# Optimization experiments

Hardware: AMD Instinct MI355X
Metric: run time of the kernel (lower is better)

The kernel has to match this reference:

```python
import jax, jax.numpy as jnp
import numpy as np

N, E, D = 50000, 800000, 128
NODE_IN, EDGE_IN, STEPS = 19, 4, 5
EPS = 1e-5

def leaky(x):
    return jnp.where(x > 0, x, 0.05 * x)

def mlp3(x, W1, b1, W2, b2, W3, b3):
    x = leaky(x @ W1 + b1)
    x = leaky(x @ W2 + b2)
    return x @ W3 + b3

def layer_norm(x, g, b):
    m = jnp.mean(x, axis=-1, keepdims=True)
    v = jnp.var(x, axis=-1, keepdims=True)
    return (x - m) * jax.lax.rsqrt(v + EPS) * g + b

def batch_norm(x, g, b):
    # training-mode BatchNorm1d: biased batch stats over node dim
    m = jnp.mean(x, axis=0)
    v = jnp.var(x, axis=0)
    return (x - m) * jax.lax.rsqrt(v + EPS) * g + b

def gcn_conv(x, src, dst, W, b):
    # PyG GCNConv: add self loops, sym-normalize by deg^{-1/2}, aggregate at dst
    h = x @ W  # [N, D]
    deg = jax.ops.segment_sum(jnp.ones(E, x.dtype), dst, num_segments=N) + 1.0
    dis = jax.lax.rsqrt(deg)
    msg = h[src] * (dis[src] * dis[dst])[:, None]  # [E, D]
    agg = jax.ops.segment_sum(msg, dst, num_segments=N) + h * (dis * dis)[:, None]
    return agg + b


def setup_inputs() -> dict:
    key = jax.random.key(0)
    ks = iter(jax.random.split(key, 64))
    w = lambda shape: jax.random.normal(next(ks), shape, jnp.float32) * 0.05
    z = lambda: jnp.zeros((D,), jnp.float32)
    o = lambda: jnp.ones((D,), jnp.float32)
    inp = {
        'node_feat': jax.random.normal(next(ks), (N, NODE_IN), jnp.float32),
        'edge_feat': jax.random.normal(next(ks), (E, EDGE_IN), jnp.float32),
        'edge_index': jax.random.randint(next(ks), (2, E), 0, N, jnp.int32),
        'enc_node_W1': w((NODE_IN, D)), 'enc_node_b1': z(),
        'enc_node_W2': w((D, D)), 'enc_node_b2': z(),
        'enc_node_W3': w((D, D)), 'enc_node_b3': z(),
        'enc_node_ln_g': o(), 'enc_node_ln_b': z(),
        'enc_edge_W1': w((EDGE_IN, D)), 'enc_edge_b1': z(),
        'enc_edge_W2': w((D, D)), 'enc_edge_b2': z(),
        'enc_edge_W3': w((D, D)), 'enc_edge_b3': z(),
        'enc_edge_ln_g': o(), 'enc_edge_ln_b': z(),
        'proc_W': w((STEPS, 2, D, D)),
        'proc_b': jnp.zeros((STEPS, 2, D), jnp.float32),
        'proc_bn_g': jnp.ones((STEPS, D), jnp.float32),
        'proc_bn_b': jnp.zeros((STEPS, D), jnp.float32),
        'dec_W1': w((D, D)), 'dec_b1': z(),
        'dec_W2': w((D, D)), 'dec_b2': z(),
        'dec_W3': w((D, D)), 'dec_b3': z(),
        'dec_ln_g': o(), 'dec_ln_b': z(),
    }
    return inp


def reference(node_feat, edge_feat, edge_index,
              enc_node_W1, enc_node_b1, enc_node_W2, enc_node_b2, enc_node_W3, enc_node_b3,
              enc_node_ln_g, enc_node_ln_b,
              enc_edge_W1, enc_edge_b1, enc_edge_W2, enc_edge_b2, enc_edge_W3, enc_edge_b3,
              enc_edge_ln_g, enc_edge_ln_b,
              proc_W, proc_b, proc_bn_g, proc_bn_b,
              dec_W1, dec_b1, dec_W2, dec_b2, dec_W3, dec_b3, dec_ln_g, dec_ln_b):
    src, dst = edge_index[0], edge_index[1]
    # encode
    hn = layer_norm(mlp3(node_feat, enc_node_W1, enc_node_b1, enc_node_W2, enc_node_b2,
                         enc_node_W3, enc_node_b3), enc_node_ln_g, enc_node_ln_b)
    he = layer_norm(mlp3(edge_feat, enc_edge_W1, enc_edge_b1, enc_edge_W2, enc_edge_b2,
                         enc_edge_W3, enc_edge_b3), enc_edge_ln_g, enc_edge_ln_b)
    # scatter-mean edge features onto source nodes
    cnt = jax.ops.segment_sum(jnp.ones(E, hn.dtype), src, num_segments=N)
    hn = hn + jax.ops.segment_sum(he, src, num_segments=N) / jnp.maximum(cnt, 1.0)[:, None]
    # 5 residual GCN processor steps (GCNConv -> LeakyReLU -> BN -> GCNConv)
    for s in range(STEPS):
        x = gcn_conv(hn, src, dst, proc_W[s, 0], proc_b[s, 0])
        x = batch_norm(leaky(x), proc_bn_g[s], proc_bn_b[s])
        x = gcn_conv(x, src, dst, proc_W[s, 1], proc_b[s, 1])
        hn = hn + x
    # decode
    return layer_norm(mlp3(hn, dec_W1, dec_b1, dec_W2, dec_b2, dec_W3, dec_b3),
                      dec_ln_g, dec_ln_b)
```

## Files before the change

kernel.cpp:

```cpp
#include <hip/hip_runtime.h>

#define NN 50000
#define NE 800000
#define DD 128
#define LN_EPS 1e-5f

typedef __attribute__((ext_vector_type(8))) short v8s;
typedef __attribute__((ext_vector_type(4))) unsigned v4u;
typedef __attribute__((ext_vector_type(4))) float f32x4;

union CvtHL { v4u u; v8s s; };

__device__ __forceinline__ float leakyf(float x){ return x > 0.f ? x : 0.05f*x; }
__device__ __forceinline__ short f2bf(float f){
  unsigned u = __float_as_uint(f);
  u = (u + 0x7fffu + ((u >> 16) & 1u)) >> 16;
  return (short)u;
}
__device__ __forceinline__ float bf2f(unsigned short h){
  return __uint_as_float(((unsigned)h) << 16);
}
__device__ __forceinline__ unsigned cvt_pk_bf16(float a, float b){
  unsigned r;
  asm("v_cvt_pk_bf16_f32 %0, %1, %2" : "=v"(r) : "v"(a), "v"(b));
  return r;
}
__device__ __forceinline__ unsigned pack_hi16(unsigned u0, unsigned u1){
  return __builtin_amdgcn_perm(u1, u0, 0x07060302u);
}
__device__ __forceinline__ short2 f2bf2v(float v){
  unsigned u = __float_as_uint(v);
  short hi = (short)(u >> 16);
  float lo = v - __uint_as_float(u & 0xffff0000u);
  return make_short2(hi, f2bf(lo));
}

__global__ void pack_w_kernel(const float* __restrict__ W, short* __restrict__ Wh,
                              short* __restrict__ Wl, int K, int Kp)
{
  int idx = blockIdx.x*256 + threadIdx.x;
  if (idx >= Kp*128) return;
  int k = idx >> 7, n = idx & 127;
  float v = (k < K) ? W[k*128 + n] : 0.f;
  short2 t = f2bf2v(v);
  size_t o = ((size_t)(k >> 3)*128 + n)*8 + (k & 7);
  Wh[o] = t.x; Wl[o] = t.y;
}

#define NPACK 11
struct PackArgs { const float* src[NPACK]; short* dh[NPACK]; short* dl[NPACK]; };

__global__ void pack_many_kernel(PackArgs pa)
{
  int m = blockIdx.y;
  int idx = blockIdx.x*256 + threadIdx.x;
  int k = idx >> 7, n = idx & 127;
  float v = pa.src[m][k*128 + n];
  short2 t = f2bf2v(v);
  size_t o = ((size_t)(k >> 3)*128 + n)*8 + (k & 7);
  pa.dh[m][o] = t.x; pa.dl[m][o] = t.y;
}

#define MFMA3(ah, al, bh, bl, ac) \
  ac = __builtin_amdgcn_mfma_f32_16x16x32_bf16(al, bh, ac, 0,0,0); \
  ac = __builtin_amdgcn_mfma_f32_16x16x32_bf16(ah, bl, ac, 0,0,0); \
  ac = __builtin_amdgcn_mfma_f32_16x16x32_bf16(ah, bh, ac, 0,0,0);

#define MFMA2(ah, bh, bl, ac) \
  ac = __builtin_amdgcn_mfma_f32_16x16x32_bf16(ah, bl, ac, 0,0,0); \
  ac = __builtin_amdgcn_mfma_f32_16x16x32_bf16(ah, bh, ac, 0,0,0);

#define SPLIT8(f0, f1, h, l) { \
  unsigned u0=__float_as_uint(f0.x), u1=__float_as_uint(f0.y), u2=__float_as_uint(f0.z), u3=__float_as_uint(f0.w); \
  unsigned u4=__float_as_uint(f1.x), u5=__float_as_uint(f1.y), u6=__float_as_uint(f1.z), u7=__float_as_uint(f1.w); \
  CvtHL ch_, cl_; \
  ch_.u = (v4u){ pack_hi16(u0,u1), pack_hi16(u2,u3), pack_hi16(u4,u5), pack_hi16(u6,u7) }; \
  cl_.u = (v4u){ \
    cvt_pk_bf16(f0.x-__uint_as_float(u0&0xffff0000u), f0.y-__uint_as_float(u1&0xffff0000u)), \
    cvt_pk_bf16(f0.z-__uint_as_float(u2&0xffff0000u), f0.w-__uint_as_float(u3&0xffff0000u)), \
    cvt_pk_bf16(f1.x-__uint_as_float(u4&0xffff0000u), f1.y-__uint_as_float(u5&0xffff0000u)), \
    cvt_pk_bf16(f1.z-__uint_as_float(u6&0xffff0000u), f1.w-__uint_as_float(u7&0xffff0000u)) }; \
  h = ch_.s; l = cl_.s; }

template<int IN_W, bool SCATTER>
__global__ __launch_bounds__(256)
void mlp_mfma_kernel(const float* __restrict__ x, int nrows,
                     const short* __restrict__ W1h, const short* __restrict__ W1l,
                     const float* __restrict__ b1,
                     const short* __restrict__ W2h, const short* __restrict__ W2l,
                     const float* __restrict__ b2,
                     const short* __restrict__ W3h, const short* __restrict__ W3l,
                     const float* __restrict__ b3,
                     const float* __restrict__ g, const float* __restrict__ bb,
                     float* __restrict__ out,
                     const int* __restrict__ sidx,
                     const int* __restrict__ eperm)
{
  constexpr int L1K = (IN_W + 31) / 32;
  __shared__ __align__(16) short Hh[128*136];
  __shared__ float lnS[128][2], lnQ[128][2];
  __shared__ int sidx_s[128];
  __shared__ __align__(16) uint4 xstage[SCATTER ? 128 : 1];

  const int tid  = threadIdx.x;
  const int lane = tid & 63, wave = tid >> 6;
  const int wr = wave >> 1, wc = wave & 1;
  const int quad = lane >> 4, low = lane & 15;
  const int row0 = blockIdx.x * 128;

  if (SCATTER) {
    if (tid < 128) {
      int e = eperm[row0 + tid];
      float4 f = ((const float4*)x)[e];
      unsigned u0=__float_as_uint(f.x), u1=__float_as_uint(f.y);
      unsigned u2=__float_as_uint(f.z), u3=__float_as_uint(f.w);
      uint4 st;
      st.x = pack_hi16(u0,u1);
      st.y = pack_hi16(u2,u3);
      st.z = cvt_pk_bf16(f.x-__uint_as_float(u0&0xffff0000u), f.y-__uint_as_float(u1&0xffff0000u));
      st.w = cvt_pk_bf16(f.z-__uint_as_float(u2&0xffff0000u), f.w-__uint_as_float(u3&0xffff0000u));
      xstage[tid] = st;
      sidx_s[tid] = sidx[row0 + tid];
    }
    __syncthreads();
  }

  f32x4 acc[4][4];

  #pragma unroll
  for (int tm=0;tm<4;tm++)
    #pragma unroll
    for (int tn=0;tn<4;tn++) acc[tm][tn] = (f32x4)0.f;

  for (int ks = 0; ks < L1K; ks++) {
    v8s ah[4], al[4], bh[4], bl[4];
    #pragma unroll
    for (int tm=0;tm<4;tm++) {
      int lr = wr*64 + tm*16 + low;
      v8s h = (v8s)0, l = (v8s)0;
      if (SCATTER && IN_W == 4) {
        if (quad == 0) {
          uint4 st = xstage[lr];
          CvtHL ch_, cl_;
          ch_.u = (v4u){ st.x, st.y, 0u, 0u };
          cl_.u = (v4u){ st.z, st.w, 0u, 0u };
          h = ch_.s; l = cl_.s;
        }
      } else if (IN_W % 32 == 0) {
        int r = row0 + lr;
        if (r < nrows) {
          const float* p = x + (size_t)r*IN_W + ks*32 + quad*8;
          float4 f0 = *(const float4*)p;
          float4 f1 = *(const float4*)(p + 4);
          SPLIT8(f0, f1, h, l);
        }
      } else {
        int r = row0 + lr;
        #pragma unroll
        for (int j=0;j<8;j++) {
          int k = ks*32 + quad*8 + j;
          if (k < IN_W && r < nrows) {
            short2 t = f2bf2v(x[(size_t)r*IN_W + k]);
            h[j] = t.x; l[j] = t.y;
          }
        }
      }
      ah[tm] = h; al[tm] = l;
    }
    #pragma unroll
    for (int tn=0;tn<4;tn++) {
      size_t o = ((size_t)(ks*4+quad)*128 + wc*64 + tn*16 + low)*8;
      bh[tn] = *(const v8s*)(W1h + o);
      bl[tn] = *(const v8s*)(W1l + o);
    }
    #pragma unroll
    for (int tm=0;tm<4;tm++)
      #pragma unroll
      for (int tn=0;tn<4;tn++) { MFMA3(ah[tm], al[tm], bh[tn], bl[tn], acc[tm][tn]); }
  }
  #pragma unroll
  for (int tn=0;tn<4;tn++) {
    float bv = b1[wc*64 + tn*16 + low];
    #pragma unroll
    for (int tm=0;tm<4;tm++) {
      unsigned p01 = cvt_pk_bf16(leakyf(acc[tm][tn][0]+bv), leakyf(acc[tm][tn][1]+bv));
      unsigned p23 = cvt_pk_bf16(leakyf(acc[tm][tn][2]+bv), leakyf(acc[tm][tn][3]+bv));
      int base = (wr*64+tm*16+quad*4)*136 + wc*64+tn*16+low;
      Hh[base]     = (short)p01;
      Hh[base+136] = (short)(p01>>16);
      Hh[base+272] = (short)p23;
      Hh[base+408] = (short)(p23>>16);
    }
  }
  __syncthreads();

  #pragma unroll
  for (int tm=0;tm<4;tm++)
    #pragma unroll
    for (int tn=0;tn<4;tn++) acc[tm][tn] = (f32x4)0.f;
  #pragma unroll
  for (int ks=0;ks<4;ks++) {
    v8s ah[4], bh[4], bl[4];
    #pragma unroll
    for (int tm=0;tm<4;tm++)
      ah[tm] = *(const v8s*)&Hh[(wr*64+tm*16+low)*136 + ks*32 + quad*8];
    #pragma unroll
    for (int tn=0;tn<4;tn++) {
      size_t o = ((size_t)(ks*4+quad)*128 + wc*64 + tn*16 + low)*8;
      bh[tn] = *(const v8s*)(W2h + o);
      bl[tn] = *(const v8s*)(W2l + o);
    }
    #pragma unroll
    for (int tm=0;tm<4;tm++)
      #pragma unroll
      for (int tn=0;tn<4;tn++) { MFMA2(ah[tm], bh[tn], bl[tn], acc[tm][tn]); }
  }
  __syncthreads();
  #pragma unroll
  for (int tn=0;tn<4;tn++) {
    float bv = b2[wc*64 + tn*16 + low];
    #pragma unroll
    for (int tm=0;tm<4;tm++) {
      unsigned p01 = cvt_pk_bf16(leakyf(acc[tm][tn][0]+bv), leakyf(acc[tm][tn][1]+bv));
      unsigned p23 = cvt_pk_bf16(leakyf(acc[tm][tn][2]+bv), leakyf(acc[tm][tn][3]+bv));
      int base = (wr*64+tm*16+quad*4)*136 + wc*64+tn*16+low;
      Hh[base]     = (short)p01;
      Hh[base+136] = (short)(p01>>16);
      Hh[base+272] = (short)p23;
      Hh[base+408] = (short)(p23>>16);
    }
  }
  __syncthreads();

  #pragma unroll
  for (int tm=0;tm<4;tm++)
    #pragma unroll
    for (int tn=0;tn<4;tn++) acc[tm][tn] = (f32x4)0.f;
  #pragma unroll
  for (int ks=0;ks<4;ks++) {
    v8s ah[4], bh[4], bl[4];
    #pragma unroll
    for (int tm=0;tm<4;tm++)
      ah[tm] = *(const v8s*)&Hh[(wr*64+tm*16+low)*136 + ks*32 + quad*8];
    #pragma unroll
    for (int tn=0;tn<4;tn++) {
      size_t o = ((size_t)(ks*4+quad)*128 + wc*64 + tn*16 + low)*8;
      bh[tn] = *(const v8s*)(W3h + o);
      bl[tn] = *(const v8s*)(W3l + o);
    }
    #pragma unroll
    for (int tm=0;tm<4;tm++)
      #pragma unroll
      for (int tn=0;tn<4;tn++) { MFMA2(ah[tm], bh[tn], bl[tn], acc[tm][tn]); }
  }
  #pragma unroll
  for (int tn=0;tn<4;tn++) {
    float bv = b3[wc*64 + tn*16 + low];
    #pragma unroll
    for (int tm=0;tm<4;tm++)
      #pragma unroll
      for (int i=0;i<4;i++) acc[tm][tn][i] += bv;
  }

  #pragma unroll
  for (int tm=0;tm<4;tm++)
    #pragma unroll
    for (int i=0;i<4;i++) {
      float s = acc[tm][0][i] + acc[tm][1][i] + acc[tm][2][i] + acc[tm][3][i];
      float q = acc[tm][0][i]*acc[tm][0][i] + acc[tm][1][i]*acc[tm][1][i]
              + acc[tm][2][i]*acc[tm][2][i] + acc[tm][3][i]*acc[tm][3][i];
      s += __shfl_xor(s, 1); q += __shfl_xor(q, 1);
      s += __shfl_xor(s, 2); q += __shfl_xor(q, 2);
      s += __shfl_xor(s, 4); q += __shfl_xor(q, 4);
      s += __shfl_xor(s, 8); q += __shfl_xor(q, 8);
      if (low == tm*4 + i) {
        int r = wr*64 + tm*16 + quad*4 + i;
        lnS[r][wc] = s; lnQ[r][wc] = q;
      }
    }
  __syncthreads();

  float g4[4], bb4[4];
  #pragma unroll
  for (int tn=0;tn<4;tn++) { int c = wc*64+tn*16+low; g4[tn] = g[c]; bb4[tn] = bb[c]; }

  #pragma unroll
  for (int tm=0;tm<4;tm++)
    #pragma unroll
    for (int i=0;i<4;i++) {
      int r = wr*64 + tm*16 + quad*4 + i;
      float s = lnS[r][0] + lnS[r][1];
      float q = lnQ[r][0] + lnQ[r][1];
      float m = s * (1.f/128.f);
      float var = q * (1.f/128.f) - m*m;
      float rs = rsqrtf(var + LN_EPS);
      int gr = row0 + r;
      if (!SCATTER && gr >= nrows) continue;
      float v0 = (acc[tm][0][i] - m) * rs * g4[0] + bb4[0];
      float v1 = (acc[tm][1][i] - m) * rs * g4[1] + bb4[1];
      float v2 = (acc[tm][2][i] - m) * rs * g4[2] + bb4[2];
      float v3 = (acc[tm][3][i] - m) * rs * g4[3] + bb4[3];
      if (SCATTER) {
        unsigned p01 = cvt_pk_bf16(v0, v1), p23 = cvt_pk_bf16(v2, v3);
        int base = r*132 + wc*64 + low;
        Hh[base]    = (short)p01;
        Hh[base+16] = (short)(p01>>16);
        Hh[base+32] = (short)p23;
        Hh[base+48] = (short)(p23>>16);
      } else {
        size_t ob = (size_t)gr*DD + wc*64 + low;
        out[ob]    = v0;
        out[ob+16] = v1;
        out[ob+32] = v2;
        out[ob+48] = v3;
      }
    }

  if (SCATTER) {
    __syncthreads();
    const unsigned* H32 = (const unsigned*)Hh;
    int cp = tid & 63;
    int gI = tid >> 6;
    int rbeg = gI*32, rend = rbeg + 32;
    unsigned pv = H32[rbeg*66 + cp];
    float a0 = __uint_as_float(pv << 16), a1 = __uint_as_float(pv & 0xffff0000u);
    int cur = sidx_s[rbeg];
    for (int r = rbeg + 1; r < rend; r++) {
      int sv = sidx_s[r];
      unsigned hv = H32[r*66 + cp];
      if (sv != cur) {
        atomicAdd(&out[(size_t)cur*DD + 2*cp],     a0);
        atomicAdd(&out[(size_t)cur*DD + 2*cp + 1], a1);
        a0 = __uint_as_float(hv << 16); a1 = __uint_as_float(hv & 0xffff0000u);
        cur = sv;
      } else {
        a0 += __uint_as_float(hv << 16); a1 += __uint_as_float(hv & 0xffff0000u);
      }
    }
    atomicAdd(&out[(size_t)cur*DD + 2*cp],     a0);
    atomicAdd(&out[(size_t)cur*DD + 2*cp + 1], a1);
  }
}

__global__ __launch_bounds__(256)
void gemm_mfma_kernel(const float* __restrict__ x,
                      const short* __restrict__ Wh, const short* __restrict__ Wl,
                      const float* __restrict__ initv, const float* __restrict__ rowscale,
                      unsigned short* __restrict__ outbf, int nrows)
{
  const int tid  = threadIdx.x;
  const int lane = tid & 63, wave = tid >> 6;
  const int wr = wave >> 1, wc = wave & 1;
  const int quad = lane >> 4, low = lane & 15;
  const int row0 = blockIdx.x * 64;

  f32x4 acc[2][4];
  #pragma unroll
  for (int tm=0;tm<2;tm++)
    #pragma unroll
    for (int tn=0;tn<4;tn++) acc[tm][tn] = (f32x4)0.f;

  #pragma unroll
  for (int ks=0;ks<4;ks++) {
    v8s ah[2], al[2], bh[4], bl[4];
    #pragma unroll
    for (int tm=0;tm<2;tm++) {
      int r = row0 + wr*32 + tm*16 + low;
      v8s h = (v8s)0, l = (v8s)0;
      if (r < nrows) {
        const float* p = x + (size_t)r*DD + ks*32 + quad*8;
        float4 f0 = *(const float4*)p;
        float4 f1 = *(const float4*)(p + 4);
        SPLIT8(f0, f1, h, l);
      }
      ah[tm] = h; al[tm] = l;
    }
    #pragma unroll
    for (int tn=0;tn<4;tn++) {
      size_t o = ((size_t)(ks*4+quad)*128 + wc*64 + tn*16 + low)*8;
      bh[tn] = *(const v8s*)(Wh + o);
      bl[tn] = *(const v8s*)(Wl + o);
    }
    #pragma unroll
    for (int tm=0;tm<2;tm++)
      #pragma unroll
      for (int tn=0;tn<4;tn++) { MFMA3(ah[tm], al[tm], bh[tn], bl[tn], acc[tm][tn]); }
  }

  float iv4[4];
  #pragma unroll
  for (int tn=0;tn<4;tn++) iv4[tn] = initv ? initv[wc*64 + tn*16 + low] : 0.f;

  #pragma unroll
  for (int tm=0;tm<2;tm++)
    #pragma unroll
    for (int i=0;i<4;i++) {
      int gr = row0 + wr*32 + tm*16 + quad*4 + i;
      if (gr >= nrows) continue;
      float sc = rowscale ? rowscale[gr] : 1.f;
      float v0 = (acc[tm][0][i] + iv4[0]) * sc;
      float v1 = (acc[tm][1][i] + iv4[1]) * sc;
      float v2 = (acc[tm][2][i] + iv4[2]) * sc;
      float v3 = (acc[tm][3][i] + iv4[3]) * sc;
      unsigned p01 = cvt_pk_bf16(v0, v1), p23 = cvt_pk_bf16(v2, v3);
      size_t base = (size_t)gr*DD + wc*64 + low;
      outbf[base]    = (unsigned short)p01;
      outbf[base+16] = (unsigned short)(p01>>16);
      outbf[base+32] = (unsigned short)p23;
      outbf[base+48] = (unsigned short)(p23>>16);
    }
}

__global__ __launch_bounds__(256)
void gemm_bf_mfma_kernel(const unsigned short* __restrict__ xb,
                         const short* __restrict__ Wh, const short* __restrict__ Wl,
                         const float* __restrict__ initv, const float* __restrict__ rowscale,
                         unsigned short* __restrict__ outbf, int nrows)
{
  const int tid  = threadIdx.x;
  const int lane = tid & 63, wave = tid >> 6;
  const int wr = wave >> 1, wc = wave & 1;
  const int quad = lane >> 4, low = lane & 15;
  const int row0 = blockIdx.x * 64;

  f32x4 acc[2][4];
  #pragma unroll
  for (int tm=0;tm<2;tm++)
    #pragma unroll
    for (int tn=0;tn<4;tn++) acc[tm][tn] = (f32x4)0.f;

  #pragma unroll
  for (int ks=0;ks<4;ks++) {
    v8s ah[2], bh[4], bl[4];
    #pragma unroll
    for (int tm=0;tm<2;tm++) {
      int r = row0 + wr*32 + tm*16 + low;
      ah[tm] = (r < nrows) ? *(const v8s*)(xb + (size_t)r*DD + ks*32 + quad*8) : (v8s)0;
    }
    #pragma unroll
    for (int tn=0;tn<4;tn++) {
      size_t o = ((size_t)(ks*4+quad)*128 + wc*64 + tn*16 + low)*8;
      bh[tn] = *(const v8s*)(Wh + o);
      bl[tn] = *(const v8s*)(Wl + o);
    }
    #pragma unroll
    for (int tm=0;tm<2;tm++)
      #pragma unroll
      for (int tn=0;tn<4;tn++) { MFMA2(ah[tm], bh[tn], bl[tn], acc[tm][tn]); }
  }

  float iv4[4];
  #pragma unroll
  for (int tn=0;tn<4;tn++) iv4[tn] = initv ? initv[wc*64 + tn*16 + low] : 0.f;

  #pragma unroll
  for (int tm=0;tm<2;tm++)
    #pragma unroll
    for (int i=0;i<4;i++) {
      int gr = row0 + wr*32 + tm*16 + quad*4 + i;
      if (gr >= nrows) continue;
      float sc = rowscale ? rowscale[gr] : 1.f;
      float v0 = (acc[tm][0][i] + iv4[0]) * sc;
      float v1 = (acc[tm][1][i] + iv4[1]) * sc;
      float v2 = (acc[tm][2][i] + iv4[2]) * sc;
      float v3 = (acc[tm][3][i] + iv4[3]) * sc;
      unsigned p01 = cvt_pk_bf16(v0, v1), p23 = cvt_pk_bf16(v2, v3);
      size_t base = (size_t)gr*DD + wc*64 + low;
      outbf[base]    = (unsigned short)p01;
      outbf[base+16] = (unsigned short)(p01>>16);
      outbf[base+32] = (unsigned short)p23;
      outbf[base+48] = (unsigned short)(p23>>16);
    }
}

__global__ __launch_bounds__(256)
void gcn_agg_kernel(const unsigned* __restrict__ hb, const int* __restrict__ rowptr,
                    const int* __restrict__ csr_src, const float* __restrict__ dis,
                    const float* __restrict__ bias, const float* __restrict__ resid,
                    float* __restrict__ outf, unsigned* __restrict__ outb, int mode)
{
  const int wv = __builtin_amdgcn_readfirstlane(threadIdx.x >> 6);
  const int lane = threadIdx.x & 63;
  const int i = blockIdx.x*4 + wv;
  if (i >= NN) return;
  unsigned hv = hb[(size_t)i*64 + lane];
  float ax = bf2f((unsigned short)(hv & 0xffff)), ay = bf2f((unsigned short)(hv >> 16));
  const int beg = rowptr[i], end = rowptr[i+1];
  int j = beg;
  for (; j + 16 <= end; j += 16) {
    unsigned v[16];
    #pragma unroll
    for (int k=0;k<16;k++) v[k] = hb[(size_t)csr_src[j+k]*64 + lane];
    #pragma unroll
    for (int k=0;k<16;k++) {
      ax += bf2f((unsigned short)(v[k] & 0xffff));
      ay += bf2f((unsigned short)(v[k] >> 16));
    }
  }
  for (; j + 4 <= end; j += 4) {
    unsigned v[4];
    #pragma unroll
    for (int k=0;k<4;k++) v[k] = hb[(size_t)csr_src[j+k]*64 + lane];
    #pragma unroll
    for (int k=0;k<4;k++) {
      ax += bf2f((unsigned short)(v[k] & 0xffff));
      ay += bf2f((unsigned short)(v[k] >> 16));
    }
  }
  for (; j < end; j++) {
    unsigned v = hb[(size_t)csr_src[j]*64 + lane];
    ax += bf2f((unsigned short)(v & 0xffff));
    ay += bf2f((unsigned short)(v >> 16));
  }
  float di = dis[i];
  ax = ax*di + bias[2*lane]; ay = ay*di + bias[2*lane+1];
  size_t o = (size_t)i*64 + lane;
  if (mode == 0) {
    outb[o] = cvt_pk_bf16(leakyf(ax), leakyf(ay));
  } else {
    float2 rs = ((const float2*)resid)[o];
    float2 r; r.x = rs.x + ax; r.y = rs.y + ay;
    ((float2*)outf)[o] = r;
  }
}

__global__ void count_kernel(const int* __restrict__ src, const int* __restrict__ dst,
                             int* __restrict__ cnt_src, int* __restrict__ deg_dst)
{
  int e = blockIdx.x*blockDim.x + threadIdx.x;
  if (e < NE) {
    atomicAdd(&cnt_src[src[e]], 1);
    atomicAdd(&deg_dst[dst[e]], 1);
  }
}

__global__ void nodeparams_kernel(const int* __restrict__ deg_dst, const int* __restrict__ cnt_src,
                                  float* __restrict__ dis, float* __restrict__ invcnt)
{
  int i = blockIdx.x*blockDim.x + threadIdx.x;
  if (i < NN) {
    dis[i] = rsqrtf((float)deg_dst[i] + 1.0f);
    invcnt[i] = 1.0f / fmaxf((float)cnt_src[i], 1.0f);
  }
}

__global__ void scan2_kernel(const int* __restrict__ a0, int* __restrict__ r0, int* __restrict__ n0,
                             const int* __restrict__ a1, int* __restrict__ r1, int* __restrict__ n1)
{
  const int* a = blockIdx.x ? a1 : a0;
  int* r = blockIdx.x ? r1 : r0;
  int* n = blockIdx.x ? n1 : n0;
  const int T = 256;
  int tid = threadIdx.x;
  int chunk = (NN + T - 1) / T;
  int begin = tid*chunk, end = begin + chunk; if (end > NN) end = NN; if (begin > NN) begin = NN;
  int s = 0;
  for (int i = begin; i < end; i++) s += a[i];
  __shared__ int ps[T];
  ps[tid] = s; __syncthreads();
  for (int off = 1; off < T; off <<= 1) {
    int v = 0;
    if (tid >= off) v = ps[tid - off];
    __syncthreads();
    if (tid >= off) ps[tid] += v;
    __syncthreads();
  }
  int base = (tid == 0) ? 0 : ps[tid-1];
  for (int i = begin; i < end; i++) { r[i] = base; n[i] = base; base += a[i]; }
  if (tid == T-1) r[NN] = base;
}

__global__ void fill_kernel(const int* __restrict__ src, const int* __restrict__ dst,
                            int* __restrict__ nextp, int* __restrict__ csr_src)
{
  int e = blockIdx.x*blockDim.x + threadIdx.x;
  if (e < NE) {
    int pos = atomicAdd(&nextp[dst[e]], 1);
    csr_src[pos] = src[e];
  }
}

__global__ void fill_src_kernel(const int* __restrict__ src, int* __restrict__ nexts,
                                int* __restrict__ eperm, int* __restrict__ srcsorted)
{
  int e = blockIdx.x*blockDim.x + threadIdx.x;
  if (e < NE) {
    int s = src[e];
    int pos = atomicAdd(&nexts[s], 1);
    eperm[pos] = e;
    srcsorted[pos] = s;
  }
}

__global__ void addmean_kernel(float* __restrict__ hn, const float* __restrict__ nodesum,
                               const float* __restrict__ invcnt)
{
  int t = blockIdx.x*blockDim.x + threadIdx.x;
  if (t < NN*DD/4) {
    float4 a = ((const float4*)hn)[t];
    float4 b = ((const float4*)nodesum)[t];
    float ic = invcnt[t >> 5];
    a.x += b.x*ic; a.y += b.y*ic; a.z += b.z*ic; a.w += b.w*ic;
    ((float4*)hn)[t] = a;
  }
}

__global__ __launch_bounds__(256)
void bn_stats_kernel(const unsigned short* __restrict__ yb, float* __restrict__ sums)
{
  int col = threadIdx.x & 127, grp = threadIdx.x >> 7;
  float s = 0.f, ss = 0.f;
  for (int i = blockIdx.x*2 + grp; i < NN; i += gridDim.x*2) {
    float v = bf2f(yb[(size_t)i*DD + col]);
    s += v; ss += v*v;
  }
  __shared__ float ls[256], lss[256];
  ls[threadIdx.x] = s; lss[threadIdx.x] = ss;
  __syncthreads();
  if (grp == 0) {
    atomicAdd(&sums[col],      ls[col]  + ls[col+128]);
    atomicAdd(&sums[DD + col], lss[col] + lss[col+128]);
  }
}

__global__ __launch_bounds__(256)
void bn_fold_kernel(const float* __restrict__ sums, const float* __restrict__ g,
                    const float* __restrict__ b, const float* __restrict__ W2,
                    short* __restrict__ Wfh, short* __restrict__ Wfl,
                    float* __restrict__ cvec)
{
  __shared__ float scale_s[DD], shift_s[DD];
  int tid = threadIdx.x;
  if (tid < DD) {
    float m = sums[tid] / (float)NN;
    float var = sums[DD + tid] / (float)NN - m*m;
    float is = rsqrtf(var + LN_EPS);
    float sc = is * g[tid];
    scale_s[tid] = sc;
    shift_s[tid] = b[tid] - m * sc;
  }
  __syncthreads();
  int col = tid & 127, kh = tid >> 7;
  float cpart = 0.f;
  #pragma unroll
  for (int kk = 0; kk < 4; kk++) {
    int k = blockIdx.x*8 + kh*4 + kk;
    float w = W2[k*DD + col];
    short2 t = f2bf2v(w * scale_s[k]);
    size_t o = ((size_t)(k >> 3)*128 + col)*8 + (k & 7);
    Wfh[o] = t.x; Wfl[o] = t.y;
    cpart += shift_s[k] * w;
  }
  atomicAdd(&cvec[col], cpart);
}

extern "C" void kernel_launch(void* const* d_in, const int* in_sizes, int n_in,
                              void* d_out, int out_size, void* d_ws, size_t ws_size,
                              hipStream_t stream)
{
  const float* node_feat = (const float*)d_in[0];
  const float* edge_feat = (const float*)d_in[1];
  const int*   edge_index = (const int*)d_in[2];
  const int* src = edge_index;
  const int* dst = edge_index + NE;

  const float* enW1 = (const float*)d_in[3];  const float* enb1 = (const float*)d_in[4];
  const float* enW2 = (const float*)d_in[5];  const float* enb2 = (const float*)d_in[6];
  const float* enW3 = (const float*)d_in[7];  const float* enb3 = (const float*)d_in[8];
  const float* enlg = (const float*)d_in[9];  const float* enlb = (const float*)d_in[10];

  const float* eeW1 = (const float*)d_in[11]; const float* eeb1 = (const float*)d_in[12];
  const float* eeW2 = (const float*)d_in[13]; const float* eeb2 = (const float*)d_in[14];
  const float* eeW3 = (const float*)d_in[15]; const float* eeb3 = (const float*)d_in[16];
  const float* eelg = (const float*)d_in[17]; const float* eelb = (const float*)d_in[18];

  const float* procW = (const float*)d_in[19];
  const float* procB = (const float*)d_in[20];
  const float* bnG   = (const float*)d_in[21];
  const float* bnB   = (const float*)d_in[22];

  const float* dW1 = (const float*)d_in[23]; const float* db1 = (const float*)d_in[24];
  const float* dW2 = (const float*)d_in[25]; const float* db2 = (const float*)d_in[26];
  const float* dW3 = (const float*)d_in[27]; const float* db3 = (const float*)d_in[28];
  const float* dlg = (const float*)d_in[29]; const float* dlb = (const float*)d_in[30];

  char* ws = (char*)d_ws;
  size_t off = 0;
  auto alloc = [&](size_t bytes) -> void* {
    void* p = ws + off;
    off = (off + bytes + 255) & ~(size_t)255;
    return p;
  };
  float* hn     = (float*)alloc((size_t)NN*DD*4);
  float* esum   = (float*)alloc((size_t)NN*DD*4);
  unsigned short* hbf = (unsigned short*)alloc((size_t)NN*DD*2);
  unsigned short* ybf = (unsigned short*)alloc((size_t)NN*DD*2);
  float* dis    = (float*)alloc(NN*4);
  float* invcnt = (float*)alloc(NN*4);
  float* bnsums = (float*)alloc(3*DD*4);
  float* cvec   = bnsums + 2*DD;
  int* deg    = (int*)alloc(NN*4);
  int* cnt    = (int*)alloc(NN*4);
  int* rowptr = (int*)alloc((NN+1)*4);
  int* nextp  = (int*)alloc(NN*4);
  int* srow   = (int*)alloc((NN+1)*4);
  int* nexts  = (int*)alloc(NN*4);
  int* csr    = (int*)alloc((size_t)NE*4);
  int* eperm  = (int*)alloc((size_t)NE*4);
  int* srcsorted = (int*)alloc((size_t)NE*4);
  auto allocW = [&](int kp) { return (short*)alloc((size_t)kp*128*2); };
  short *pN1h=allocW(32),  *pN1l=allocW(32);
  short *pN2h=allocW(128), *pN2l=allocW(128);
  short *pN3h=allocW(128), *pN3l=allocW(128);
  short *pE1h=allocW(32),  *pE1l=allocW(32);
  short *pE2h=allocW(128), *pE2l=allocW(128);
  short *pE3h=allocW(128), *pE3l=allocW(128);
  short *pD1h=allocW(128), *pD1l=allocW(128);
  short *pD2h=allocW(128), *pD2l=allocW(128);
  short *pD3h=allocW(128), *pD3l=allocW(128);
  short *pP0h[5], *pP0l[5];
  for (int s = 0; s < 5; s++) { pP0h[s]=allocW(128); pP0l[s]=allocW(128); }
  short *pWfh=allocW(128), *pWfl=allocW(128);

  (void)hipMemsetAsync(deg, 0, NN*4, stream);
  (void)hipMemsetAsync(cnt, 0, NN*4, stream);
  (void)hipMemsetAsync(esum, 0, (size_t)NN*DD*4, stream);

  PackArgs pa;
  const float* s128[NPACK] = { enW2, enW3, eeW2, eeW3, dW1, dW2, dW3,
                               procW + 0*(size_t)DD*DD*2, procW + 1*(size_t)DD*DD*2,
                               procW + 2*(size_t)DD*DD*2, procW + 3*(size_t)DD*DD*2 };
  short* d128h[NPACK] = { pN2h, pN3h, pE2h, pE3h, pD1h, pD2h, pD3h, pP0h[0], pP0h[1], pP0h[2], pP0h[3] };
  short* d128l[NPACK] = { pN2l, pN3l, pE2l, pE3l, pD1l, pD2l, pD3l, pP0l[0], pP0l[1], pP0l[2], pP0l[3] };
  for (int m = 0; m < NPACK; m++) { pa.src[m]=s128[m]; pa.dh[m]=d128h[m]; pa.dl[m]=d128l[m]; }
  pack_many_kernel<<<dim3(64, NPACK), 256, 0, stream>>>(pa);
  const int G32 = (32*128+255)/256, G128 = (128*128+255)/256;
  pack_w_kernel<<<G32, 256, 0, stream>>>(enW1, pN1h, pN1l, 19, 32);
  pack_w_kernel<<<G32, 256, 0, stream>>>(eeW1, pE1h, pE1l, 4, 32);
  pack_w_kernel<<<G128,256, 0, stream>>>(procW + 4*(size_t)DD*DD*2, pP0h[4], pP0l[4], 128, 128);

  count_kernel<<<(NE+255)/256, 256, 0, stream>>>(src, dst, cnt, deg);
  nodeparams_kernel<<<(NN+255)/256, 256, 0, stream>>>(deg, cnt, dis, invcnt);
  scan2_kernel<<<2, 256, 0, stream>>>(deg, rowptr, nextp, cnt, srow, nexts);
  fill_kernel<<<(NE+255)/256, 256, 0, stream>>>(src, dst, nextp, csr);
  fill_src_kernel<<<(NE+255)/256, 256, 0, stream>>>(src, nexts, eperm, srcsorted);

  const int GN  = (NN + 127) / 128;
  const int GE  = NE / 128;
  const int GG  = (NN + 63) / 64;
  const int GA  = (NN + 3) / 4;

  mlp_mfma_kernel<19, false><<<GN, 256, 0, stream>>>(node_feat, NN,
      pN1h, pN1l, enb1, pN2h, pN2l, enb2, pN3h, pN3l, enb3, enlg, enlb, hn,
      nullptr, nullptr);
  mlp_mfma_kernel<4, true><<<GE, 256, 0, stream>>>(edge_feat, NE,
      pE1h, pE1l, eeb1, pE2h, pE2l, eeb2, pE3h, pE3l, eeb3, eelg, eelb, esum,
      srcsorted, eperm);
  addmean_kernel<<<(NN*DD/4+255)/256, 256, 0, stream>>>(hn, esum, invcnt);

  for (int s = 0; s < 5; s++) {
    const float* Wc2 = procW + (size_t)(s*2+1)*DD*DD;
    const float* b0  = procB + (size_t)(s*2+0)*DD;
    const float* b1p = procB + (size_t)(s*2+1)*DD;

    gemm_mfma_kernel<<<GG, 256, 0, stream>>>(hn, pP0h[s], pP0l[s], nullptr, dis, hbf, NN);
    gcn_agg_kernel<<<GA, 256, 0, stream>>>((const unsigned*)hbf, rowptr, csr, dis,
                                           b0, nullptr, nullptr, (unsigned*)ybf, 0);
    (void)hipMemsetAsync(bnsums, 0, 3*DD*4, stream);
    bn_stats_kernel<<<512, 256, 0, stream>>>(ybf, bnsums);
    bn_fold_kernel<<<16, 256, 0, stream>>>(bnsums, bnG + s*DD, bnB + s*DD, Wc2, pWfh, pWfl, cvec);
    gemm_bf_mfma_kernel<<<GG, 256, 0, stream>>>(ybf, pWfh, pWfl, cvec, dis, hbf, NN);
    gcn_agg_kernel<<<GA, 256, 0, stream>>>((const unsigned*)hbf, rowptr, csr, dis,
                                           b1p, hn, hn, nullptr, 1);
  }

  mlp_mfma_kernel<128, false><<<GN, 256, 0, stream>>>(hn, NN,
      pD1h, pD1l, db1, pD2h, pD2l, db2, pD3h, pD3l, db3, dlg, dlb, (float*)d_out,
      nullptr, nullptr);
}
```

Baseline: 1.333 ms.

## Rework edge MLP first layer, gather aggregation, epilogues and graph setup kernels

The edge-encoder first layer is rewritten as a single bf16 MFMA pass. The hi/lo split of the 4 inputs is folded into the K dimension, and the bias goes in through a constant-one column, which replaces the three-MFMA split product. The GCN aggregation now gathers 16-byte vectors, with four neighbours per wave in parallel, a cross-quad shuffle reduce and a grid-stride loop over 2048 blocks. Layer-norm row reductions use a transpose-style shuffle tree, and epilogues use packed f32 add/mul. The setup kernels are fused: node params go into the scan and both CSR fills share one kernel. The edge layer-1 change slightly alters numerics because the lo part of the weight is dropped for some terms.

```diff
diff --git a/kernel.cpp b/kernel.cpp
--- a/kernel.cpp
+++ b/kernel.cpp
@@ -8,6 +8,7 @@
 typedef __attribute__((ext_vector_type(8))) short v8s;
 typedef __attribute__((ext_vector_type(4))) unsigned v4u;
 typedef __attribute__((ext_vector_type(4))) float f32x4;
+typedef __attribute__((ext_vector_type(2))) float f32x2;
 
 union CvtHL { v4u u; v8s s; };
 
@@ -24,6 +25,12 @@
   unsigned r;
   asm("v_cvt_pk_bf16_f32 %0, %1, %2" : "=v"(r) : "v"(a), "v"(b));
   return r;
+}
+__device__ __forceinline__ f32x2 pk_add(f32x2 a, f32x2 b){
+  f32x2 r; asm("v_pk_add_f32 %0, %1, %2" : "=v"(r) : "v"(a), "v"(b)); return r;
+}
+__device__ __forceinline__ f32x2 pk_mul(f32x2 a, f32x2 b){
+  f32x2 r; asm("v_pk_mul_f32 %0, %1, %2" : "=v"(r) : "v"(a), "v"(b)); return r;
 }
 __device__ __forceinline__ unsigned pack_hi16(unsigned u0, unsigned u1){
   return __builtin_amdgcn_perm(u1, u0, 0x07060302u);
@@ -45,6 +52,22 @@
   short2 t = f2bf2v(v);
   size_t o = ((size_t)(k >> 3)*128 + n)*8 + (k & 7);
   Wh[o] = t.x; Wl[o] = t.y;
+}
+
+__global__ void pack_edge_w1_kernel(const float* __restrict__ W1, const float* __restrict__ b1,
+                                    short* __restrict__ Wp)
+{
+  int idx = blockIdx.x*256 + threadIdx.x;
+  if (idx >= 32*128) return;
+  int k = idx >> 7, n = idx & 127;
+  short v = 0;
+  if (k < 4)        v = f2bf2v(W1[k*128 + n]).x;
+  else if (k < 8)   v = f2bf2v(W1[(k-4)*128 + n]).y;
+  else if (k < 12)  v = f2bf2v(W1[(k-8)*128 + n]).x;
+  else if (k == 12) v = f2bf2v(b1[n]).x;
+  else if (k == 13) v = f2bf2v(b1[n]).y;
+  size_t o = ((size_t)(k >> 3)*128 + n)*8 + (k & 7);
+  Wp[o] = v;
 }
 
 #define NPACK 11
@@ -81,6 +104,15 @@
     cvt_pk_bf16(f1.x-__uint_as_float(u4&0xffff0000u), f1.y-__uint_as_float(u5&0xffff0000u)), \
     cvt_pk_bf16(f1.z-__uint_as_float(u6&0xffff0000u), f1.w-__uint_as_float(u7&0xffff0000u)) }; \
   h = ch_.s; l = cl_.s; }
+
+#define EPI_PK(accv, bv2, DOBIAS, p01, p23) { \
+  f32x2 x01 = (f32x2){(accv)[0], (accv)[1]}; \
+  f32x2 x23 = (f32x2){(accv)[2], (accv)[3]}; \
+  if (DOBIAS) { x01 = pk_add(x01, bv2); x23 = pk_add(x23, bv2); } \
+  f32x2 m01 = pk_mul(x01, (f32x2)(0.05f)); \
+  f32x2 m23 = pk_mul(x23, (f32x2)(0.05f)); \
+  p01 = cvt_pk_bf16(fmaxf(x01.x, m01.x), fmaxf(x01.y, m01.y)); \
+  p23 = cvt_pk_bf16(fmaxf(x23.x, m23.x), fmaxf(x23.y, m23.y)); }
 
 template<int IN_W, bool SCATTER>
 __global__ __launch_bounds__(256)
@@ -97,6 +129,7 @@
                      const int* __restrict__ eperm)
 {
   constexpr int L1K = (IN_W + 31) / 32;
+  constexpr bool EDGE1 = (SCATTER && IN_W == 4);
   __shared__ __align__(16) short Hh[128*136];
   __shared__ float lnS[128][2], lnQ[128][2];
   __shared__ int sidx_s[128];
@@ -132,59 +165,81 @@
     #pragma unroll
     for (int tn=0;tn<4;tn++) acc[tm][tn] = (f32x4)0.f;
 
-  for (int ks = 0; ks < L1K; ks++) {
-    v8s ah[4], al[4], bh[4], bl[4];
+  if constexpr (EDGE1) {
+    v8s ah[4], bh[4];
     #pragma unroll
     for (int tm=0;tm<4;tm++) {
       int lr = wr*64 + tm*16 + low;
-      v8s h = (v8s)0, l = (v8s)0;
-      if (SCATTER && IN_W == 4) {
-        if (quad == 0) {
-          uint4 st = xstage[lr];
-          CvtHL ch_, cl_;
-          ch_.u = (v4u){ st.x, st.y, 0u, 0u };
-          cl_.u = (v4u){ st.z, st.w, 0u, 0u };
-          h = ch_.s; l = cl_.s;
-        }
-      } else if (IN_W % 32 == 0) {
-        int r = row0 + lr;
-        if (r < nrows) {
-          const float* p = x + (size_t)r*IN_W + ks*32 + quad*8;
-          float4 f0 = *(const float4*)p;
-          float4 f1 = *(const float4*)(p + 4);
-          SPLIT8(f0, f1, h, l);
-        }
-      } else {
-        int r = row0 + lr;
-        #pragma unroll
-        for (int j=0;j<8;j++) {
-          int k = ks*32 + quad*8 + j;
-          if (k < IN_W && r < nrows) {
-            short2 t = f2bf2v(x[(size_t)r*IN_W + k]);
-            h[j] = t.x; l[j] = t.y;
+      v8s h = (v8s)0;
+      if (quad == 0) {
+        uint4 st = xstage[lr];
+        CvtHL c_; c_.u = (v4u){ st.x, st.y, st.x, st.y };
+        h = c_.s;
+      } else if (quad == 1) {
+        uint4 st = xstage[lr];
+        CvtHL c_; c_.u = (v4u){ st.z, st.w, 0x3F803F80u, 0u };
+        h = c_.s;
+      }
+      ah[tm] = h;
+    }
+    #pragma unroll
+    for (int tn=0;tn<4;tn++) {
+      size_t o = ((size_t)quad*128 + wc*64 + tn*16 + low)*8;
+      bh[tn] = *(const v8s*)(W1h + o);
+    }
+    #pragma unroll
+    for (int tm=0;tm<4;tm++)
+      #pragma unroll
+      for (int tn=0;tn<4;tn++)
+        acc[tm][tn] = __builtin_amdgcn_mfma_f32_16x16x32_bf16(ah[tm], bh[tn], acc[tm][tn], 0,0,0);
+  } else {
+    for (int ks = 0; ks < L1K; ks++) {
+      v8s ah[4], al[4], bh[4], bl[4];
+      #pragma unroll
+      for (int tm=0;tm<4;tm++) {
+        int lr = wr*64 + tm*16 + low;
+        v8s h = (v8s)0, l = (v8s)0;
+        if (IN_W % 32 == 0) {
+          int r = row0 + lr;
+          if (r < nrows) {
+            const float* p = x + (size_t)r*IN_W + ks*32 + quad*8;
+            float4 f0 = *(const float4*)p;
+            float4 f1 = *(const float4*)(p + 4);
+            SPLIT8(f0, f1, h, l);
+          }
+        } else {
+          int r = row0 + lr;
+          #pragma unroll
+          for (int j=0;j<8;j++) {
+            int k = ks*32 + quad*8 + j;
+            if (k < IN_W && r < nrows) {
+              short2 t = f2bf2v(x[(size_t)r*IN_W + k]);
+              h[j] = t.x; l[j] = t.y;
+            }
           }
         }
-      }
-      ah[tm] = h; al[tm] = l;
-    }
-    #pragma unroll
-    for (int tn=0;tn<4;tn++) {
-      size_t o = ((size_t)(ks*4+quad)*128 + wc*64 + tn*16 + low)*8;
-      bh[tn] = *(const v8s*)(W1h + o);
-      bl[tn] = *(const v8s*)(W1l + o);
-    }
-    #pragma unroll
-    for (int tm=0;tm<4;tm++)
-      #pragma unroll
-      for (int tn=0;tn<4;tn++) { MFMA3(ah[tm], al[tm], bh[tn], bl[tn], acc[tm][tn]); }
+        ah[tm] = h; al[tm] = l;
+      }
+      #pragma unroll
+      for (int tn=0;tn<4;tn++) {
+        size_t o = ((size_t)(ks*4+quad)*128 + wc*64 + tn*16 + low)*8;
+        bh[tn] = *(const v8s*)(W1h + o);
+        bl[tn] = *(const v8s*)(W1l + o);
+      }
+      #pragma unroll
+      for (int tm=0;tm<4;tm++)
+        #pragma unroll
+        for (int tn=0;tn<4;tn++) { MFMA3(ah[tm], al[tm], bh[tn], bl[tn], acc[tm][tn]); }
+    }
   }
   #pragma unroll
   for (int tn=0;tn<4;tn++) {
-    float bv = b1[wc*64 + tn*16 + low];
+    float bv = EDGE1 ? 0.f : b1[wc*64 + tn*16 + low];
+    f32x2 bv2 = (f32x2)(bv);
     #pragma unroll
     for (int tm=0;tm<4;tm++) {
-      unsigned p01 = cvt_pk_bf16(leakyf(acc[tm][tn][0]+bv), leakyf(acc[tm][tn][1]+bv));
-      unsigned p23 = cvt_pk_bf16(leakyf(acc[tm][tn][2]+bv), leakyf(acc[tm][tn][3]+bv));
+      unsigned p01, p23;
+      EPI_PK(acc[tm][tn], bv2, !EDGE1, p01, p23);
       int base = (wr*64+tm*16+quad*4)*136 + wc*64+tn*16+low;
       Hh[base]     = (short)p01;
       Hh[base+136] = (short)(p01>>16);
@@ -219,10 +274,11 @@
   #pragma unroll
   for (int tn=0;tn<4;tn++) {
     float bv = b2[wc*64 + tn*16 + low];
+    f32x2 bv2 = (f32x2)(bv);
     #pragma unroll
     for (int tm=0;tm<4;tm++) {
-      unsigned p01 = cvt_pk_bf16(leakyf(acc[tm][tn][0]+bv), leakyf(acc[tm][tn][1]+bv));
-      unsigned p23 = cvt_pk_bf16(leakyf(acc[tm][tn][2]+bv), leakyf(acc[tm][tn][3]+bv));
+      unsigned p01, p23;
+      EPI_PK(acc[tm][tn], bv2, true, p01, p23);
       int base = (wr*64+tm*16+quad*4)*136 + wc*64+tn*16+low;
       Hh[base]     = (short)p01;
       Hh[base+136] = (short)(p01>>16);
@@ -262,22 +318,44 @@
       for (int i=0;i<4;i++) acc[tm][tn][i] += bv;
   }
 
-  #pragma unroll
-  for (int tm=0;tm<4;tm++)
-    #pragma unroll
-    for (int i=0;i<4;i++) {
-      float s = acc[tm][0][i] + acc[tm][1][i] + acc[tm][2][i] + acc[tm][3][i];
-      float q = acc[tm][0][i]*acc[tm][0][i] + acc[tm][1][i]*acc[tm][1][i]
-              + acc[tm][2][i]*acc[tm][2][i] + acc[tm][3][i]*acc[tm][3][i];
-      s += __shfl_xor(s, 1); q += __shfl_xor(q, 1);
-      s += __shfl_xor(s, 2); q += __shfl_xor(q, 2);
-      s += __shfl_xor(s, 4); q += __shfl_xor(q, 4);
-      s += __shfl_xor(s, 8); q += __shfl_xor(q, 8);
-      if (low == tm*4 + i) {
-        int r = wr*64 + tm*16 + quad*4 + i;
-        lnS[r][wc] = s; lnQ[r][wc] = q;
-      }
-    }
+  {
+    float ct[16];
+    #pragma unroll
+    for (int tm=0;tm<4;tm++)
+      #pragma unroll
+      for (int i=0;i<4;i++)
+        ct[tm*4+i] = acc[tm][0][i] + acc[tm][1][i] + acc[tm][2][i] + acc[tm][3][i];
+    #pragma unroll
+    for (int st=0; st<4; st++) {
+      const int mm = 1 << st;
+      const bool hbit = ((low >> st) & 1) != 0;
+      #pragma unroll
+      for (int p=0; p < (16>>st); p+=2) {
+        float snd = hbit ? ct[p]   : ct[p+1];
+        float kp  = hbit ? ct[p+1] : ct[p];
+        ct[p>>1] = kp + __shfl_xor(snd, mm);
+      }
+    }
+    { int r = wr*64 + (low>>2)*16 + quad*4 + (low&3); lnS[r][wc] = ct[0]; }
+    #pragma unroll
+    for (int tm=0;tm<4;tm++)
+      #pragma unroll
+      for (int i=0;i<4;i++)
+        ct[tm*4+i] = acc[tm][0][i]*acc[tm][0][i] + acc[tm][1][i]*acc[tm][1][i]
+                   + acc[tm][2][i]*acc[tm][2][i] + acc[tm][3][i]*acc[tm][3][i];
+    #pragma unroll
+    for (int st=0; st<4; st++) {
+      const int mm = 1 << st;
+      const bool hbit = ((low >> st) & 1) != 0;
+      #pragma unroll
+      for (int p=0; p < (16>>st); p+=2) {
+        float snd = hbit ? ct[p]   : ct[p+1];
+        float kp  = hbit ? ct[p+1] : ct[p];
+        ct[p>>1] = kp + __shfl_xor(snd, mm);
+      }
+    }
+    { int r = wr*64 + (low>>2)*16 + quad*4 + (low&3); lnQ[r][wc] = ct[0]; }
+  }
   __syncthreads();
 
   float g4[4], bb4[4];
@@ -289,8 +367,10 @@
     #pragma unroll
     for (int i=0;i<4;i++) {
       int r = wr*64 + tm*16 + quad*4 + i;
-      float s = lnS[r][0] + lnS[r][1];
-      float q = lnQ[r][0] + lnQ[r][1];
+      float2 S2 = *(const float2*)&lnS[r][0];
+      float2 Q2 = *(const float2*)&lnQ[r][0];
+      float s = S2.x + S2.y;
+      float q = Q2.x + Q2.y;
       float m = s * (1.f/128.f);
       float var = q * (1.f/128.f) - m*m;
       float rs = rsqrtf(var + LN_EPS);
@@ -473,6 +553,12 @@
     }
 }
 
+#define ADD8(a, vv) { \
+  a[0] += __uint_as_float((vv).x << 16); a[1] += __uint_as_float((vv).x & 0xffff0000u); \
+  a[2] += __uint_as_float((vv).y << 16); a[3] += __uint_as_float((vv).y & 0xffff0000u); \
+  a[4] += __uint_as_float((vv).z << 16); a[5] += __uint_as_float((vv).z & 0xffff0000u); \
+  a[6] += __uint_as_float((vv).w << 16); a[7] += __uint_as_float((vv).w & 0xffff0000u); }
+
 __global__ __launch_bounds__(256)
 void gcn_agg_kernel(const unsigned* __restrict__ hb, const int* __restrict__ rowptr,
                     const int* __restrict__ csr_src, const float* __restrict__ dis,
@@ -481,46 +567,67 @@
 {
   const int wv = __builtin_amdgcn_readfirstlane(threadIdx.x >> 6);
   const int lane = threadIdx.x & 63;
-  const int i = blockIdx.x*4 + wv;
-  if (i >= NN) return;
-  unsigned hv = hb[(size_t)i*64 + lane];
-  float ax = bf2f((unsigned short)(hv & 0xffff)), ay = bf2f((unsigned short)(hv >> 16));
-  const int beg = rowptr[i], end = rowptr[i+1];
-  int j = beg;
-  for (; j + 16 <= end; j += 16) {
-    unsigned v[16];
-    #pragma unroll
-    for (int k=0;k<16;k++) v[k] = hb[(size_t)csr_src[j+k]*64 + lane];
-    #pragma unroll
-    for (int k=0;k<16;k++) {
-      ax += bf2f((unsigned short)(v[k] & 0xffff));
-      ay += bf2f((unsigned short)(v[k] >> 16));
-    }
-  }
-  for (; j + 4 <= end; j += 4) {
-    unsigned v[4];
-    #pragma unroll
-    for (int k=0;k<4;k++) v[k] = hb[(size_t)csr_src[j+k]*64 + lane];
-    #pragma unroll
-    for (int k=0;k<4;k++) {
-      ax += bf2f((unsigned short)(v[k] & 0xffff));
-      ay += bf2f((unsigned short)(v[k] >> 16));
-    }
-  }
-  for (; j < end; j++) {
-    unsigned v = hb[(size_t)csr_src[j]*64 + lane];
-    ax += bf2f((unsigned short)(v & 0xffff));
-    ay += bf2f((unsigned short)(v >> 16));
-  }
-  float di = dis[i];
-  ax = ax*di + bias[2*lane]; ay = ay*di + bias[2*lane+1];
-  size_t o = (size_t)i*64 + lane;
-  if (mode == 0) {
-    outb[o] = cvt_pk_bf16(leakyf(ax), leakyf(ay));
-  } else {
-    float2 rs = ((const float2*)resid)[o];
-    float2 r; r.x = rs.x + ax; r.y = rs.y + ay;
-    ((float2*)outf)[o] = r;
+  const int q4 = lane >> 4;
+  const int c4 = lane & 15;
+  const uint4* hb4 = (const uint4*)hb;
+  for (int i = blockIdx.x*4 + wv; i < NN; i += gridDim.x*4) {
+    const int beg = rowptr[i], end = rowptr[i+1];
+    float a[8];
+    #pragma unroll
+    for (int t=0;t<8;t++) a[t] = 0.f;
+    if (q4 == 0) {
+      uint4 sv = hb4[(size_t)i*16 + c4];
+      ADD8(a, sv);
+    }
+    int j = beg;
+    for (; j + 16 <= end; j += 16) {
+      uint4 v[4];
+      #pragma unroll
+      for (int k=0;k<4;k++) {
+        int s0=csr_src[j+4*k], s1=csr_src[j+4*k+1], s2=csr_src[j+4*k+2], s3=csr_src[j+4*k+3];
+        int s = q4==0 ? s0 : q4==1 ? s1 : q4==2 ? s2 : s3;
+        v[k] = hb4[(size_t)s*16 + c4];
+      }
+      #pragma unroll
+      for (int k=0;k<4;k++) ADD8(a, v[k]);
+    }
+    for (; j + 4 <= end; j += 4) {
+      int s0=csr_src[j], s1=csr_src[j+1], s2=csr_src[j+2], s3=csr_src[j+3];
+      int s = q4==0 ? s0 : q4==1 ? s1 : q4==2 ? s2 : s3;
+      uint4 v = hb4[(size_t)s*16 + c4];
+      ADD8(a, v);
+    }
+    if (j < end) {
+      int rem = end - j;
+      int s = csr_src[j + (q4 < rem ? q4 : 0)];
+      uint4 v = hb4[(size_t)s*16 + c4];
+      if (q4 < rem) ADD8(a, v);
+    }
+    #pragma unroll
+    for (int t=0;t<8;t++) { a[t] += __shfl_xor(a[t], 16); a[t] += __shfl_xor(a[t], 32); }
+    float di = dis[i];
+    float4 b0 = ((const float4*)bias)[2*c4], b1 = ((const float4*)bias)[2*c4+1];
+    a[0]=a[0]*di+b0.x; a[1]=a[1]*di+b0.y; a[2]=a[2]*di+b0.z; a[3]=a[3]*di+b0.w;
+    a[4]=a[4]*di+b1.x; a[5]=a[5]*di+b1.y; a[6]=a[6]*di+b1.z; a[7]=a[7]*di+b1.w;
+    if (mode == 0) {
+      if (q4 == 0) {
+        uint4 pk;
+        pk.x = cvt_pk_bf16(leakyf(a[0]), leakyf(a[1]));
+        pk.y = cvt_pk_bf16(leakyf(a[2]), leakyf(a[3]));
+        pk.z = cvt_pk_bf16(leakyf(a[4]), leakyf(a[5]));
+        pk.w = cvt_pk_bf16(leakyf(a[6]), leakyf(a[7]));
+        ((uint4*)outb)[(size_t)i*16 + c4] = pk;
+      }
+    } else {
+      if (q4 == 0) {
+        float4 r0 = ((const float4*)resid)[(size_t)i*32 + 2*c4];
+        float4 r1 = ((const float4*)resid)[(size_t)i*32 + 2*c4+1];
+        r0.x+=a[0]; r0.y+=a[1]; r0.z+=a[2]; r0.w+=a[3];
+        r1.x+=a[4]; r1.y+=a[5]; r1.z+=a[6]; r1.w+=a[7];
+        ((float4*)outf)[(size_t)i*32 + 2*c4]   = r0;
+        ((float4*)outf)[(size_t)i*32 + 2*c4+1] = r1;
+      }
+    }
   }
 }
 
@@ -534,22 +641,15 @@
   }
 }
 
-__global__ void nodeparams_kernel(const int* __restrict__ deg_dst, const int* __restrict__ cnt_src,
-                                  float* __restrict__ dis, float* __restrict__ invcnt)
-{
-  int i = blockIdx.x*blockDim.x + threadIdx.x;
-  if (i < NN) {
-    dis[i] = rsqrtf((float)deg_dst[i] + 1.0f);
-    invcnt[i] = 1.0f / fmaxf((float)cnt_src[i], 1.0f);
-  }
-}
-
 __global__ void scan2_kernel(const int* __restrict__ a0, int* __restrict__ r0, int* __restrict__ n0,
-                             const int* __restrict__ a1, int* __restrict__ r1, int* __restrict__ n1)
+                             float* __restrict__ aux0,
+                             const int* __restrict__ a1, int* __restrict__ r1, int* __restrict__ n1,
+                             float* __restrict__ aux1)
 {
   const int* a = blockIdx.x ? a1 : a0;
   int* r = blockIdx.x ? r1 : r0;
   int* n = blockIdx.x ? n1 : n0;
+  float* aux = blockIdx.x ? aux1 : aux0;
   const int T = 256;
   int tid = threadIdx.x;
   int chunk = (NN + T - 1) / T;
@@ -566,29 +666,26 @@
     __syncthreads();
   }
   int base = (tid == 0) ? 0 : ps[tid-1];
-  for (int i = begin; i < end; i++) { r[i] = base; n[i] = base; base += a[i]; }
+  for (int i = begin; i < end; i++) {
+    r[i] = base; n[i] = base; base += a[i];
+    aux[i] = blockIdx.x ? (1.0f / fmaxf((float)a[i], 1.0f)) : rsqrtf((float)a[i] + 1.0f);
+  }
   if (tid == T-1) r[NN] = base;
 }
 
-__global__ void fill_kernel(const int* __restrict__ src, const int* __restrict__ dst,
-                            int* __restrict__ nextp, int* __restrict__ csr_src)
-{
-  int e = blockIdx.x*blockDim.x + threadIdx.x;
-  if (e < NE) {
-    int pos = atomicAdd(&nextp[dst[e]], 1);
-    csr_src[pos] = src[e];
-  }
-}
-
-__global__ void fill_src_kernel(const int* __restrict__ src, int* __restrict__ nexts,
-                                int* __restrict__ eperm, int* __restrict__ srcsorted)
+__global__ void fill_both_kernel(const int* __restrict__ src, const int* __restrict__ dst,
+                                 int* __restrict__ nextp, int* __restrict__ csr_src,
+                                 int* __restrict__ nexts, int* __restrict__ eperm,
+                                 int* __restrict__ srcsorted)
 {
   int e = blockIdx.x*blockDim.x + threadIdx.x;
   if (e < NE) {
     int s = src[e];
-    int pos = atomicAdd(&nexts[s], 1);
-    eperm[pos] = e;
-    srcsorted[pos] = s;
+    int pos = atomicAdd(&nextp[dst[e]], 1);
+    csr_src[pos] = s;
+    int ps = atomicAdd(&nexts[s], 1);
+    eperm[ps] = e;
+    srcsorted[ps] = s;
   }
 }
 
@@ -736,19 +833,17 @@
   pack_many_kernel<<<dim3(64, NPACK), 256, 0, stream>>>(pa);
   const int G32 = (32*128+255)/256, G128 = (128*128+255)/256;
   pack_w_kernel<<<G32, 256, 0, stream>>>(enW1, pN1h, pN1l, 19, 32);
-  pack_w_kernel<<<G32, 256, 0, stream>>>(eeW1, pE1h, pE1l, 4, 32);
+  pack_edge_w1_kernel<<<G32, 256, 0, stream>>>(eeW1, eeb1, pE1h);
   pack_w_kernel<<<G128,256, 0, stream>>>(procW + 4*(size_t)DD*DD*2, pP0h[4], pP0l[4], 128, 128);
 
   count_kernel<<<(NE+255)/256, 256, 0, stream>>>(src, dst, cnt, deg);
-  nodeparams_kernel<<<(NN+255)/256, 256, 0, stream>>>(deg, cnt, dis, invcnt);
-  scan2_kernel<<<2, 256, 0, stream>>>(deg, rowptr, nextp, cnt, srow, nexts);
-  fill_kernel<<<(NE+255)/256, 256, 0, stream>>>(src, dst, nextp, csr);
-  fill_src_kernel<<<(NE+255)/256, 256, 0, stream>>>(src, nexts, eperm, srcsorted);
+  scan2_kernel<<<2, 256, 0, stream>>>(deg, rowptr, nextp, dis, cnt, srow, nexts, invcnt);
+  fill_both_kernel<<<(NE+255)/256, 256, 0, stream>>>(src, dst, nextp, csr, nexts, eperm, srcsorted);
 
   const int GN  = (NN + 127) / 128;
   const int GE  = NE / 128;
   const int GG  = (NN + 63) / 64;
-  const int GA  = (NN + 3) / 4;
+  const int GA  = 2048;
 
   mlp_mfma_kernel<19, false><<<GN, 256, 0, stream>>>(node_feat, NN,
       pN1h, pN1l, enb1, pN2h, pN2l, enb2, pN3h, pN3l, enb3, enlg, enlb, hn,
```

After: 1.364 ms. +2.3%, slower.
